# Optimization experiments

Measured on AMD Instinct MI355X. Metric: run time of the kernel, lower is better.

The kernel has to match this reference:

```python
import jax, jax.numpy as jnp
import numpy as np

# ---- static hyperparameters (from init_kwargs) ----
N_ORDER = 3
P = N_ORDER + 1                      # nodes per element
N_ELEM = 64
N_NODES = N_ELEM * N_ORDER + 1       # 193
XMIN_IN, XMAX_IN = -1.0, 1.0         # inner layer domain
XMIN_OUT, XMAX_OUT = -3.0, 3.0       # outer layer domain (covers t_ik range)
N_SAMPLES, N_WIDTH, NDIM = 32768, 32, 4

_NODES = np.linspace(-1.0, 1.0, P)   # reference-element nodes


def lagr_bases(xt):
    """Lagrange basis values and 1st/2nd derivatives on the reference element.
    xt: (...,) -> phi, dphi, ddphi each (..., P)."""
    nd = _NODES
    d = xt[..., None] - jnp.asarray(nd, dtype=xt.dtype)  # (..., P), d[...,m] = x - nodes[m]
    phi_l, dphi_l, ddphi_l = [], [], []
    for j in range(P):
        # phi_j = prod_{m!=j} (x - n_m)/(n_j - n_m)
        p = jnp.ones_like(xt)
        for m in range(P):
            if m != j:
                p = p * d[..., m] / float(nd[j] - nd[m])
        phi_l.append(p)
        # dphi_j = sum_{i!=j} 1/(n_j-n_i) * prod_{m!=i,j} (x-n_m)/(n_j-n_m)
        y = jnp.zeros_like(xt)
        for i in range(P):
            if i == j:
                continue
            k = jnp.ones_like(xt) / float(nd[j] - nd[i])
            for m in range(P):
                if m != i and m != j:
                    k = k * d[..., m] / float(nd[j] - nd[m])
            y = y + k
        dphi_l.append(y)
        # ddphi_j = sum_{i!=j} 1/(n_j-n_i) * sum_{m!=i,j} 1/(n_j-n_m) * prod_{n!=i,j,m} (x-n_n)/(n_j-n_n)
        y2 = jnp.zeros_like(xt)
        for i in range(P):
            if i == j:
                continue
            ks = jnp.zeros_like(xt)
            for m in range(P):
                if m == i or m == j:
                    continue
                kp = jnp.ones_like(xt) / float(nd[j] - nd[m])
                for n in range(P):
                    if n != i and n != j and n != m:
                        kp = kp * d[..., n] / float(nd[j] - nd[n])
                ks = ks + kp
            y2 = y2 + ks / float(nd[j] - nd[i])
        ddphi_l.append(y2)
    return (jnp.stack(phi_l, -1), jnp.stack(dphi_l, -1), jnp.stack(ddphi_l, -1))


def layer_transform(x, x_min, x_max, n_nodes, n_elements):
    """Shift to natural coords, pick element by floor-division, map to reference coords."""
    x_shift = (n_nodes - 1) * (x - x_min) / (x_max - x_min)
    id_el = jnp.clip(jnp.floor(x_shift / N_ORDER), 0.0, n_elements - 1)
    nodes_l = (id_el * N_ORDER).astype(jnp.int32)
    x_ref = 2.0 * (x_shift - nodes_l) / N_ORDER - 1.0
    delta = 0.5 * N_ORDER * (x_max - x_min) / (n_nodes - 1)
    return x_ref, nodes_l, delta


def setup_inputs() -> dict:
    key = jax.random.key(0)
    k1, k2, k3 = jax.random.split(key, 3)
    x = jax.random.uniform(k1, (N_SAMPLES, NDIM), dtype=jnp.float32)       # in [x_min, x_max]
    W_in = 0.1 * jax.random.normal(k2, (N_WIDTH, N_NODES, NDIM), dtype=jnp.float32)
    W_out = 0.1 * jax.random.normal(k3, (N_WIDTH, N_NODES), dtype=jnp.float32)
    return {"x": x, "W_in": W_in, "W_out": W_out}


def reference(x, W_in, W_out):
    I, J = x.shape
    K = W_in.shape[0]
    # ---- inner layer: per-(sample,width,dim) local Lagrange basis ----
    xk = jnp.broadcast_to(x[:, None, :], (I, K, J))                        # (I,K,J)
    xt, nodes_l, delta = layer_transform(xk, XMIN_IN, XMAX_IN, N_NODES, N_ELEM)
    phi, dphi, ddphi = lagr_bases(xt)                                      # (I,K,J,P)
    # gather form of scatter + einsum('kpj,ikpj->ik'): sum_p,j W[k, nodes_l+p, j]*phi_local
    node_idx = nodes_l[..., None] + jnp.arange(P)                          # (I,K,J,P)
    kk = jnp.arange(K)[None, :, None, None]
    jj = jnp.arange(J)[None, None, :, None]
    Wg = W_in[kk, node_idx, jj]                                            # (I,K,J,P)
    t = jnp.einsum('ikjp,ikjp->ik', Wg, phi)
    dt = jnp.einsum('ikjp,ikjp->ik', Wg, dphi) / delta
    ddt = jnp.einsum('ikjp,ikjp->ik', Wg, ddphi) / (delta * delta)
    # ---- outer layer on t_ik (already 2D) ----
    xt2, nodes_l2, _ = layer_transform(t, XMIN_OUT, XMAX_OUT, N_NODES, N_ELEM)
    phi2, _, _ = lagr_bases(xt2)                                           # (I,K,P)
    node_idx2 = nodes_l2[..., None] + jnp.arange(P)                        # (I,K,P)
    kk2 = jnp.arange(K)[None, :, None]
    W2g = W_out[kk2, node_idx2]                                            # (I,K,P)
    y = jnp.einsum('ikp,ikp->ik', W2g, phi2)
    return jnp.stack([y, t, dt, ddt], axis=0)                              # (4,I,K)
```

## Files before the change

kernel.cpp:

```cpp
#include <hip/hip_runtime.h>

constexpr int I_SAMPLES = 32768;
constexpr int K_WIDTH   = 32;
constexpr int NNODES    = 193;
constexpr int IK        = I_SAMPLES * K_WIDTH;

__global__ __launch_bounds__(256) void kann_kernel(
    const float* __restrict__ x,
    const float* __restrict__ W_in,
    const float* __restrict__ W_out,
    float* __restrict__ out)
{
    const int tid = blockIdx.x * blockDim.x + threadIdx.x;
    const int k = tid & 31;
    const int i = tid >> 5;

    const float4 xv = reinterpret_cast<const float4*>(x)[i];
    const float xj[4] = {xv.x, xv.y, xv.z, xv.w};

    const float C3[4] = {-0.5625f,  1.6875f, -1.6875f,  0.5625f};
    const float C2[4] = { 0.5625f, -0.5625f, -0.5625f,  0.5625f};
    const float C1[4] = { 0.0625f, -1.6875f,  1.6875f, -0.0625f};
    const float C0[4] = {-0.0625f,  0.5625f,  0.5625f, -0.0625f};

    float t = 0.f, dta = 0.f, dda = 0.f;
    const float* Wk = W_in + k * (NNODES * 4);

    #pragma unroll
    for (int j = 0; j < 4; ++j) {
        const float xs = (192.0f * (xj[j] + 1.0f)) / 2.0f;
        float ide = floorf(xs / 3.0f);
        ide = fminf(fmaxf(ide, 0.0f), 63.0f);
        const int nl = (int)(ide * 3.0f);
        const float xr = (2.0f * (xs - (float)nl)) / 3.0f - 1.0f;

        #pragma unroll
        for (int p = 0; p < 4; ++p) {
            const float w     = Wk[(nl + p) * 4 + j];
            const float phi   = ((C3[p] * xr + C2[p]) * xr + C1[p]) * xr + C0[p];
            const float dphi  = (3.0f * C3[p] * xr + 2.0f * C2[p]) * xr + C1[p];
            const float ddphi = 6.0f * C3[p] * xr + 2.0f * C2[p];
            t   += w * phi;
            dta += w * dphi;
            dda += w * ddphi;
        }
    }
    const float dt  = dta * 64.0f;
    const float ddt = dda * 4096.0f;

    const float xs2 = (192.0f * (t + 3.0f)) / 6.0f;
    float id2 = floorf(xs2 / 3.0f);
    id2 = fminf(fmaxf(id2, 0.0f), 63.0f);
    const int nl2 = (int)(id2 * 3.0f);
    const float xr2 = (2.0f * (xs2 - (float)nl2)) / 3.0f - 1.0f;

    float y = 0.f;
    const float* Wo = W_out + k * NNODES + nl2;
    #pragma unroll
    for (int p = 0; p < 4; ++p) {
        const float phi = ((C3[p] * xr2 + C2[p]) * xr2 + C1[p]) * xr2 + C0[p];
        y += Wo[p] * phi;
    }

    out[tid]          = y;
    out[IK + tid]     = t;
    out[2 * IK + tid] = dt;
    out[3 * IK + tid] = ddt;
}

extern "C" void kernel_launch(void* const* d_in, const int* in_sizes, int n_in,
                              void* d_out, int out_size, void* d_ws, size_t ws_size,
                              hipStream_t stream) {
    const float* x     = (const float*)d_in[0];
    const float* W_in  = (const float*)d_in[1];
    const float* W_out = (const float*)d_in[2];
    float* out = (float*)d_out;

    dim3 grid(IK / 256), block(256);
    kann_kernel<<<grid, block, 0, stream>>>(x, W_in, W_out, out);
}
```

Measured before the change: 84.73 us.

## Repack weights per element into float4 tables with k-contiguous layout

Adds a prep kernel that gathers the four node weights of each element into a float4, stored as [j][element][k] for W_in and [element][k] for W_out. The main kernel then does one 16-byte load per dimension instead of four strided scalar loads, and lanes with the same element read adjacent addresses. The cost is an extra kernel launch and workspace traffic on every call, which is small next to the output writes.

```diff
diff --git a/kernel.cpp b/kernel.cpp
--- a/kernel.cpp
+++ b/kernel.cpp
@@ -3,12 +3,48 @@
 constexpr int I_SAMPLES = 32768;
 constexpr int K_WIDTH   = 32;
 constexpr int NNODES    = 193;
+constexpr int N_ELEM    = 64;
 constexpr int IK        = I_SAMPLES * K_WIDTH;
+
+constexpr int W1_N = 4 * N_ELEM * K_WIDTH;
+constexpr int W2_N = N_ELEM * K_WIDTH;
+
+__global__ __launch_bounds__(256) void prep_kernel(
+    const float* __restrict__ W_in,
+    const float* __restrict__ W_out,
+    float4* __restrict__ W1,
+    float4* __restrict__ W2)
+{
+    const int t = blockIdx.x * blockDim.x + threadIdx.x;
+    if (t < W1_N) {
+        const int k = t & 31;
+        const int e = (t >> 5) & 63;
+        const int j = t >> 11;
+        const int base = (k * NNODES + 3 * e) * 4 + j;
+        float4 v;
+        v.x = W_in[base + 0 * 4];
+        v.y = W_in[base + 1 * 4];
+        v.z = W_in[base + 2 * 4];
+        v.w = W_in[base + 3 * 4];
+        W1[t] = v;
+    } else if (t < W1_N + W2_N) {
+        const int u = t - W1_N;
+        const int k = u & 31;
+        const int e = u >> 5;
+        const int base = k * NNODES + 3 * e;
+        float4 v;
+        v.x = W_out[base + 0];
+        v.y = W_out[base + 1];
+        v.z = W_out[base + 2];
+        v.w = W_out[base + 3];
+        W2[u] = v;
+    }
+}
 
 __global__ __launch_bounds__(256) void kann_kernel(
     const float* __restrict__ x,
-    const float* __restrict__ W_in,
-    const float* __restrict__ W_out,
+    const float4* __restrict__ W1,
+    const float4* __restrict__ W2,
     float* __restrict__ out)
 {
     const int tid = blockIdx.x * blockDim.x + threadIdx.x;
@@ -24,25 +60,27 @@
     const float C0[4] = {-0.0625f,  0.5625f,  0.5625f, -0.0625f};
 
     float t = 0.f, dta = 0.f, dda = 0.f;
-    const float* Wk = W_in + k * (NNODES * 4);
 
     #pragma unroll
     for (int j = 0; j < 4; ++j) {
         const float xs = (192.0f * (xj[j] + 1.0f)) / 2.0f;
         float ide = floorf(xs / 3.0f);
         ide = fminf(fmaxf(ide, 0.0f), 63.0f);
-        const int nl = (int)(ide * 3.0f);
+        const int e  = (int)ide;
+        const int nl = 3 * e;
         const float xr = (2.0f * (xs - (float)nl)) / 3.0f - 1.0f;
+
+        const float4 w = W1[(j * N_ELEM + e) * K_WIDTH + k];
+        const float wv[4] = {w.x, w.y, w.z, w.w};
 
         #pragma unroll
         for (int p = 0; p < 4; ++p) {
-            const float w     = Wk[(nl + p) * 4 + j];
             const float phi   = ((C3[p] * xr + C2[p]) * xr + C1[p]) * xr + C0[p];
             const float dphi  = (3.0f * C3[p] * xr + 2.0f * C2[p]) * xr + C1[p];
             const float ddphi = 6.0f * C3[p] * xr + 2.0f * C2[p];
-            t   += w * phi;
-            dta += w * dphi;
-            dda += w * ddphi;
+            t   += wv[p] * phi;
+            dta += wv[p] * dphi;
+            dda += wv[p] * ddphi;
         }
     }
     const float dt  = dta * 64.0f;
@@ -51,15 +89,17 @@
     const float xs2 = (192.0f * (t + 3.0f)) / 6.0f;
     float id2 = floorf(xs2 / 3.0f);
     id2 = fminf(fmaxf(id2, 0.0f), 63.0f);
-    const int nl2 = (int)(id2 * 3.0f);
+    const int e2  = (int)id2;
+    const int nl2 = 3 * e2;
     const float xr2 = (2.0f * (xs2 - (float)nl2)) / 3.0f - 1.0f;
 
+    const float4 w2 = W2[e2 * K_WIDTH + k];
+    const float w2v[4] = {w2.x, w2.y, w2.z, w2.w};
     float y = 0.f;
-    const float* Wo = W_out + k * NNODES + nl2;
     #pragma unroll
     for (int p = 0; p < 4; ++p) {
         const float phi = ((C3[p] * xr2 + C2[p]) * xr2 + C1[p]) * xr2 + C0[p];
-        y += Wo[p] * phi;
+        y += w2v[p] * phi;
     }
 
     out[tid]          = y;
@@ -76,6 +116,9 @@
     const float* W_out = (const float*)d_in[2];
     float* out = (float*)d_out;
 
-    dim3 grid(IK / 256), block(256);
-    kann_kernel<<<grid, block, 0, stream>>>(x, W_in, W_out, out);
+    float4* W1 = (float4*)d_ws;
+    float4* W2 = W1 + W1_N;
+
+    prep_kernel<<<(W1_N + W2_N + 255) / 256, 256, 0, stream>>>(W_in, W_out, W1, W2);
+    kann_kernel<<<IK / 256, 256, 0, stream>>>(x, W1, W2, out);
 }
```

Result: faster. 72.08 us (-14.9%).
